# Performance work log

Measured on AMD Instinct MI355X. Metric: run time of the kernel, lower is better.

## Reference

```python
import jax, jax.numpy as jnp
import numpy as np

N_NODES = 50000
N_EDGES = 800000
IN_FEATS = 256
H_FEATS = 256
NUM_CLASSES = 16
NUM_GRAPHS = 64


def _glorot(key, shape):
    lim = float(np.sqrt(6.0 / (shape[0] + shape[1])))
    return jax.random.uniform(key, shape, jnp.float32, -lim, lim)


def setup_inputs() -> dict:
    key = jax.random.key(0)
    ks = jax.random.split(key, 12)
    x = jax.random.normal(ks[0], (N_NODES, IN_FEATS), jnp.float32)
    edge_index = jax.random.randint(ks[1], (2, N_EDGES), 0, N_NODES, jnp.int64)
    batch_vec = jnp.sort(jax.random.randint(ks[2], (N_NODES,), 0, NUM_GRAPHS, jnp.int64))
    W1 = _glorot(ks[3], (IN_FEATS, H_FEATS)); b1 = jnp.zeros((H_FEATS,), jnp.float32)
    W2 = _glorot(ks[4], (H_FEATS, H_FEATS)); b2 = jnp.zeros((H_FEATS,), jnp.float32)
    W3 = _glorot(ks[5], (H_FEATS, H_FEATS)); b3 = jnp.zeros((H_FEATS,), jnp.float32)
    W4 = _glorot(ks[6], (H_FEATS, NUM_CLASSES)); b4 = jnp.zeros((NUM_CLASSES,), jnp.float32)
    return {"x": x, "edge_index": edge_index, "batch_vec": batch_vec,
            "W1": W1, "b1": b1, "W2": W2, "b2": b2,
            "W3": W3, "b3": b3, "W4": W4, "b4": b4}


def gcn_conv(x, W, b, src, dst, deg_inv_sqrt):
    # PyG GCNConv: out = D^{-1/2} (A + I) D^{-1/2} (x W) + b
    h = x @ W  # [N, F_out]
    norm = deg_inv_sqrt[src] * deg_inv_sqrt[dst]  # [E+N]
    msgs = h[src] * norm[:, None]  # gather + scale
    agg = jax.ops.segment_sum(msgs, dst, num_segments=x.shape[0])
    return agg + b


def reference(x, edge_index, batch_vec, W1, b1, W2, b2, W3, b3, W4, b4):
    n = x.shape[0]
    # add self-loops once (shared across layers)
    loops = jnp.arange(n, dtype=edge_index.dtype)
    src = jnp.concatenate([edge_index[0], loops])
    dst = jnp.concatenate([edge_index[1], loops])
    deg = jax.ops.segment_sum(jnp.ones_like(dst, dtype=x.dtype), dst, num_segments=n)
    deg_inv_sqrt = jnp.where(deg > 0, jax.lax.rsqrt(deg), 0.0)

    h = gcn_conv(x, W1, b1, src, dst, deg_inv_sqrt)
    h_copy = jax.nn.relu(h)
    # dropout is identity in eval mode (training=False)
    h = gcn_conv(h_copy, W2, b2, src, dst, deg_inv_sqrt)
    h_copy = jax.nn.relu(jax.nn.relu(h) + h_copy)
    h = gcn_conv(h_copy, W3, b3, src, dst, deg_inv_sqrt)
    h = jax.nn.relu(jax.nn.relu(h) + h_copy)
    h = gcn_conv(h, W4, b4, src, dst, deg_inv_sqrt)

    # global_mean_pool over batch vector
    sums = jax.ops.segment_sum(h, batch_vec, num_segments=NUM_GRAPHS)
    counts = jax.ops.segment_sum(jnp.ones((n,), h.dtype), batch_vec, num_segments=NUM_GRAPHS)
    return sums / jnp.maximum(counts, 1.0)[:, None]
```

## Files before the change

kernel.cpp:

```cpp
#include <hip/hip_runtime.h>
#include <hip/hip_bf16.h>

#define N_NODES 50000
#define N_EDGES 800000
#define F 256
#define NGRAPH 64
#define NCLS 16
#define NBLK_N 196

typedef short short8 __attribute__((ext_vector_type(8)));
typedef float f32x4 __attribute__((ext_vector_type(4)));

__device__ __forceinline__ float bf2f(ushort u) {
    unsigned v = ((unsigned)u) << 16;
    return __uint_as_float(v);
}
__device__ __forceinline__ ushort f2bf(float f) {
    __hip_bfloat16 b = __float2bfloat16(f);
    return *reinterpret_cast<ushort*>(&b);
}
__device__ __forceinline__ float bflo(uint u) { return __uint_as_float(u << 16); }
__device__ __forceinline__ float bfhi(uint u) { return __uint_as_float(u & 0xffff0000u); }


__global__ __launch_bounds__(256) void k_init(int* __restrict__ ecnt,
                                              float* __restrict__ pool,
                                              float* __restrict__ cnt) {
    int i = blockIdx.x * 256 + threadIdx.x;
    if (i < N_NODES) ecnt[i] = 0;
    if (i < NGRAPH * NCLS) pool[i] = 0.f;
    if (i < NGRAPH) cnt[i] = 0.f;
}

__global__ __launch_bounds__(256) void k_count(const int* __restrict__ dst,
                                               int* __restrict__ ecnt) {
    int e = blockIdx.x * 256 + threadIdx.x;
    if (e < N_EDGES) atomicAdd(&ecnt[dst[e]], 1);
}

__global__ __launch_bounds__(256) void k_scan_block(const int* __restrict__ ecnt,
                                                    int* __restrict__ rowptr,
                                                    int* __restrict__ blkSum,
                                                    float* __restrict__ dinv,
                                                    float* __restrict__ sdeg) {
    __shared__ int sh[256];
    int i = blockIdx.x * 256 + threadIdx.x;
    int v = (i < N_NODES) ? ecnt[i] : 0;
    sh[threadIdx.x] = v;
    __syncthreads();
#pragma unroll
    for (int off = 1; off < 256; off <<= 1) {
        int t = (threadIdx.x >= off) ? sh[threadIdx.x - off] : 0;
        __syncthreads();
        sh[threadIdx.x] += t;
        __syncthreads();
    }
    if (i < N_NODES) {
        rowptr[i] = sh[threadIdx.x] - v;
        float d = (float)(v + 1);
        dinv[i] = rsqrtf(d);
        sdeg[i] = sqrtf(d);
    }
    if (threadIdx.x == 255) blkSum[blockIdx.x] = sh[255];
}

__global__ __launch_bounds__(256) void k_scan_add(const int* __restrict__ blkSum,
                                                  int* __restrict__ rowptr,
                                                  int* __restrict__ cursor) {
    __shared__ int sh[256];
    int t = threadIdx.x;
    sh[t] = (t < NBLK_N && t < (int)blockIdx.x) ? blkSum[t] : 0;
    __syncthreads();
#pragma unroll
    for (int off = 128; off > 0; off >>= 1) {
        if (t < off) sh[t] += sh[t + off];
        __syncthreads();
    }
    int base = sh[0];
    int i = blockIdx.x * 256 + t;
    if (i < N_NODES) {
        int r = rowptr[i] + base;
        rowptr[i] = r;
        cursor[i] = r;
    }
    if (i == 0) rowptr[N_NODES] = N_EDGES;
}

__global__ __launch_bounds__(256) void k_fill_csr(const int* __restrict__ src,
                                                  const int* __restrict__ dst,
                                                  int* __restrict__ cursor,
                                                  ushort* __restrict__ csr16) {
    int e = blockIdx.x * 256 + threadIdx.x;
    if (e >= N_EDGES) return;
    int s = src[e];
    int d = dst[e];
    int p = atomicAdd(&cursor[d], 1);
    csr16[p] = (ushort)s;
}


__global__ __launch_bounds__(256) void k_prescale(const float* __restrict__ x,
                                                  const float* __restrict__ dinv,
                                                  ushort* __restrict__ T0) {
    int i = blockIdx.x * 256 + threadIdx.x;
    if (i >= (int)((size_t)N_NODES * F / 8)) return;
    int n = i >> 5;
    float di = dinv[n];
    const float4* ip = (const float4*)(x + (size_t)i * 8);
    float4 a = ip[0], b = ip[1];
    short8 v;
    v[0] = (short)f2bf(a.x * di); v[1] = (short)f2bf(a.y * di);
    v[2] = (short)f2bf(a.z * di); v[3] = (short)f2bf(a.w * di);
    v[4] = (short)f2bf(b.x * di); v[5] = (short)f2bf(b.y * di);
    v[6] = (short)f2bf(b.z * di); v[7] = (short)f2bf(b.w * di);
    *(short8*)(T0 + (size_t)i * 8) = v;
}


__global__ __launch_bounds__(256) void k_wpack3(const float* __restrict__ W1,
                                                const float* __restrict__ W2,
                                                const float* __restrict__ W3,
                                                ushort* __restrict__ Wp) {
    int gid = blockIdx.x * 256 + threadIdx.x;
    int which = gid >> 13;
    int idx = gid & 8191;
    const float* W = (which == 0) ? W1 : (which == 1) ? W2 : W3;
    ushort* o = Wp + (size_t)which * 65536;
    int lane = idx & 63;
    int ks = (idx >> 6) & 7;
    int ctg = idx >> 9;
    int kbase = ks * 32 + (lane >> 4) * 8;
    int col = ctg * 16 + (lane & 15);
    short8 v;
#pragma unroll
    for (int e = 0; e < 8; ++e)
        v[e] = (short)f2bf(W[(size_t)(kbase + e) * 256 + col]);
    *(short8*)(o + (size_t)idx * 8) = v;
}


template <int MODE>
__global__ __launch_bounds__(256) void k_layer(const ushort* __restrict__ Hs,
                                               const ushort* __restrict__ Wp,
                                               const float* __restrict__ bias,
                                               const float* __restrict__ dinv,
                                               const float* __restrict__ sdeg,
                                               const int* __restrict__ rowptr,
                                               const ushort* __restrict__ csr16,
                                               ushort* __restrict__ OUT) {
    __shared__ __align__(16) ushort At[16 * 264];
    __shared__ __align__(16) ushort cs[4][16 * 72];
    const int t = threadIdx.x;
    const int wv = t >> 6;
    const int l = t & 63;
    const int m0 = blockIdx.x * 16;

    {
        const int slot = l >> 5;
        const int c = (l & 31) * 8;
#pragma unroll
        for (int rep = 0; rep < 4; ++rep) {
            const int noderow = wv * 4 + rep;
            const int n = m0 + noderow;
            const bool valid = n < N_NODES;
            const int nn = valid ? n : 0;

            float acc[8];
#pragma unroll
            for (int j = 0; j < 8; ++j) acc[j] = 0.f;

            int i = valid ? rowptr[nn] + slot : 0;
            const int end = valid ? rowptr[nn + 1] : 0;
            for (; i + 6 < end; i += 8) {
                int s0 = csr16[i], s1 = csr16[i + 2], s2 = csr16[i + 4], s3 = csr16[i + 6];
                short8 v0 = *(const short8*)(Hs + (size_t)s0 * F + c);
                short8 v1 = *(const short8*)(Hs + (size_t)s1 * F + c);
                short8 v2 = *(const short8*)(Hs + (size_t)s2 * F + c);
                short8 v3 = *(const short8*)(Hs + (size_t)s3 * F + c);
#pragma unroll
                for (int j = 0; j < 8; ++j)
                    acc[j] += (bf2f((ushort)v0[j]) + bf2f((ushort)v1[j])) +
                              (bf2f((ushort)v2[j]) + bf2f((ushort)v3[j]));
            }
            for (; i < end; i += 2) {
                int s0 = csr16[i];
                short8 v0 = *(const short8*)(Hs + (size_t)s0 * F + c);
#pragma unroll
                for (int j = 0; j < 8; ++j) acc[j] += bf2f((ushort)v0[j]);
            }

#pragma unroll
            for (int j = 0; j < 8; ++j) acc[j] += __shfl_xor(acc[j], 32);

            if (slot == 0) {
                short8 av;
                if (valid) {
                    const short8 h = *(const short8*)(Hs + (size_t)nn * F + c);
                    float di = dinv[nn];
#pragma unroll
                    for (int j = 0; j < 8; ++j)
                        av[j] = (short)f2bf(di * (acc[j] + bf2f((ushort)h[j])));
                } else {
#pragma unroll
                    for (int j = 0; j < 8; ++j) av[j] = 0;
                }
                *(short8*)&At[noderow * 264 + c] = av;
            }
        }
    }
    __syncthreads();

    const int colbase = wv * 64;
    const int lrow = l & 15;
    const int lk = (l >> 4) * 8;
    const short8* wp = (const short8*)Wp;

    short8 af[8];
#pragma unroll
    for (int ks = 0; ks < 8; ++ks)
        af[ks] = *(const short8*)&At[lrow * 264 + lk + ks * 32];

#pragma unroll
    for (int ct = 0; ct < 4; ++ct) {
        short8 wf[8];
#pragma unroll
        for (int ks = 0; ks < 8; ++ks)
            wf[ks] = wp[(size_t)(((wv * 4 + ct) * 8 + ks) * 64) + l];

        f32x4 acc = (f32x4){0.f, 0.f, 0.f, 0.f};
#pragma unroll
        for (int ks = 0; ks < 8; ++ks)
            acc = __builtin_amdgcn_mfma_f32_16x16x32_bf16(af[ks], wf[ks], acc, 0, 0, 0);

        int col = ct * 16 + (l & 15);
#pragma unroll
        for (int r = 0; r < 4; ++r) {
            int row = (l >> 4) * 4 + r;
            cs[wv][row * 72 + col] = f2bf(acc[r]);
        }
    }
#pragma unroll
    for (int h = 0; h < 2; ++h) {
        int row = h * 8 + (l >> 3);
        int coff = (l & 7) * 8;
        int orow = m0 + row;
        if (orow < N_NODES) {
            short8 z8 = *(const short8*)&cs[wv][row * 72 + coff];
            int gcol = colbase + coff;
            const float4 b0 = *(const float4*)(bias + gcol);
            const float4 b1 = *(const float4*)(bias + gcol + 4);
            float bb[8] = {b0.x, b0.y, b0.z, b0.w, b1.x, b1.y, b1.z, b1.w};
            float di = dinv[orow];
            short8 ov;
            if (MODE == 2) {
                const short8 hp = *(const short8*)(Hs + (size_t)orow * F + gcol);
                float sd = sdeg[orow];
#pragma unroll
                for (int j = 0; j < 8; ++j) {
                    float u = fmaxf(bf2f((ushort)z8[j]) + bb[j], 0.f);
                    u = fmaxf(u + bf2f((ushort)hp[j]) * sd, 0.f);
                    ov[j] = (short)f2bf(u * di);
                }
            } else {
#pragma unroll
                for (int j = 0; j < 8; ++j) {
                    float u = fmaxf(bf2f((ushort)z8[j]) + bb[j], 0.f);
                    ov[j] = (short)f2bf(u * di);
                }
            }
            *(short8*)(OUT + (size_t)orow * F + gcol) = ov;
        }
    }
}


__global__ __launch_bounds__(256) void k_gemm16(const ushort* __restrict__ A,
                                                const float* __restrict__ W4,
                                                ushort* __restrict__ C) {
    __shared__ float Ws[256][16];
    const int t = threadIdx.x;
    {
        const float4* wp = (const float4*)(W4 + (size_t)t * 16);
        float4 a = wp[0], b = wp[1], c = wp[2], d = wp[3];
        float4* sp = (float4*)&Ws[t][0];
        sp[0] = a; sp[1] = b; sp[2] = c; sp[3] = d;
    }
    __syncthreads();
    int row = blockIdx.x * 256 + t;
    if (row >= N_NODES) return;
    const short8* ap = (const short8*)(A + (size_t)row * F);
    float acc[16];
#pragma unroll
    for (int c = 0; c < 16; ++c) acc[c] = 0.f;
    for (int k8 = 0; k8 < 32; ++k8) {
        short8 a8 = ap[k8];
#pragma unroll
        for (int j = 0; j < 8; ++j) {
            float av = bf2f((ushort)a8[j]);
            const float4* wr = (const float4*)&Ws[k8 * 8 + j][0];
            float4 w0 = wr[0], w1 = wr[1], w2 = wr[2], w3 = wr[3];
            acc[0]  += av * w0.x; acc[1]  += av * w0.y;
            acc[2]  += av * w0.z; acc[3]  += av * w0.w;
            acc[4]  += av * w1.x; acc[5]  += av * w1.y;
            acc[6]  += av * w1.z; acc[7]  += av * w1.w;
            acc[8]  += av * w2.x; acc[9]  += av * w2.y;
            acc[10] += av * w2.z; acc[11] += av * w2.w;
            acc[12] += av * w3.x; acc[13] += av * w3.y;
            acc[14] += av * w3.z; acc[15] += av * w3.w;
        }
    }
    short8 o0, o1;
#pragma unroll
    for (int c = 0; c < 8; ++c) o0[c] = (short)f2bf(acc[c]);
#pragma unroll
    for (int c = 0; c < 8; ++c) o1[c] = (short)f2bf(acc[8 + c]);
    short8* op = (short8*)(C + (size_t)row * 16);
    op[0] = o0; op[1] = o1;
}


__global__ __launch_bounds__(256) void k_g16pool(const ushort* __restrict__ G16,
                                                 const float* __restrict__ bias,
                                                 const float* __restrict__ dinv,
                                                 const int* __restrict__ rowptr,
                                                 const ushort* __restrict__ csr16,
                                                 const int* __restrict__ batch,
                                                 float* __restrict__ pool,
                                                 float* __restrict__ cnt) {
    __shared__ float ps[NGRAPH][NCLS];
    __shared__ float pc[NGRAPH];
    for (int i = threadIdx.x; i < NGRAPH * NCLS; i += 256) ((float*)ps)[i] = 0.f;
    if (threadIdx.x < NGRAPH) pc[threadIdx.x] = 0.f;
    __syncthreads();

    int gid = blockIdx.x * 256 + threadIdx.x;
    int n = gid >> 2;
    int q = (gid & 3) * 4;
    if (n < N_NODES) {
        float ax = 0.f, ay = 0.f, az = 0.f, aw = 0.f;
        const int end = rowptr[n + 1];
        for (int i = rowptr[n]; i < end; ++i) {
            int s0 = csr16[i];
            const uint2 u = *(const uint2*)(G16 + (size_t)s0 * 16 + q);
            ax += bflo(u.x); ay += bfhi(u.x);
            az += bflo(u.y); aw += bfhi(u.y);
        }
        const uint2 hu = *(const uint2*)(G16 + (size_t)n * 16 + q);
        const float4 b = *(const float4*)(bias + q);
        float di = dinv[n];
        int g = batch[n];
        atomicAdd(&ps[g][q + 0], b.x + di * (ax + bflo(hu.x)));
        atomicAdd(&ps[g][q + 1], b.y + di * (ay + bfhi(hu.x)));
        atomicAdd(&ps[g][q + 2], b.z + di * (az + bflo(hu.y)));
        atomicAdd(&ps[g][q + 3], b.w + di * (aw + bfhi(hu.y)));
        if ((gid & 3) == 0) atomicAdd(&pc[g], 1.f);
    }
    __syncthreads();

    for (int i = threadIdx.x; i < NGRAPH * NCLS; i += 256) {
        float v = ((float*)ps)[i];
        if (v != 0.f) unsafeAtomicAdd(&pool[i], v);
    }
    if (threadIdx.x < NGRAPH) {
        float v = pc[threadIdx.x];
        if (v > 0.f) unsafeAtomicAdd(&cnt[threadIdx.x], v);
    }
}

__global__ __launch_bounds__(256) void k_final(const float* __restrict__ pool,
                                               const float* __restrict__ cnt,
                                               float* __restrict__ out) {
    int i = blockIdx.x * 256 + threadIdx.x;
    if (i < NGRAPH * NCLS) out[i] = pool[i] / fmaxf(cnt[i >> 4], 1.f);
}


extern "C" void kernel_launch(void* const* d_in, const int* in_sizes, int n_in,
                              void* d_out, int out_size, void* d_ws, size_t ws_size,
                              hipStream_t stream) {
    const float* x   = (const float*)d_in[0];
    const int*   ei  = (const int*)d_in[1];
    const int*   bvec= (const int*)d_in[2];
    const float* W1  = (const float*)d_in[3];
    const float* b1  = (const float*)d_in[4];
    const float* W2  = (const float*)d_in[5];
    const float* b2  = (const float*)d_in[6];
    const float* W3  = (const float*)d_in[7];
    const float* b3  = (const float*)d_in[8];
    const float* W4  = (const float*)d_in[9];
    const float* b4  = (const float*)d_in[10];
    float* out = (float*)d_out;

    const int* src = ei;
    const int* dst = ei + N_EDGES;

    const size_t NF = (size_t)N_NODES * F;
    ushort* T0  = (ushort*)d_ws;
    ushort* T1  = T0 + NF;
    ushort* T2  = T1 + NF;
    ushort* G16 = T2 + NF;
    float*  aux = (float*)(G16 + (size_t)N_NODES * 16 + 64);
    int*    ecnt   = (int*)aux;
    float*  dinv   = aux + N_NODES;
    float*  sdeg   = aux + 2 * N_NODES;
    int*    rowptr = (int*)(aux + 3 * N_NODES);
    int*    cursor = (int*)(aux + 4 * N_NODES + 64);
    int*    blkSum = (int*)(aux + 5 * N_NODES + 64);
    ushort* csr16  = (ushort*)(blkSum + 256);
    float*  pool   = (float*)(csr16 + N_EDGES);
    float*  cnt    = pool + NGRAPH * NCLS;
    ushort* Wp     = (ushort*)(cnt + NGRAPH);

    const int BN = NBLK_N;
    const int BE = (N_EDGES + 255) / 256;
    const int BL = (N_NODES + 15) / 16;
    const int B4 = (N_NODES * 4 + 255) / 256;
    const int BP = (int)((NF / 8 + 255) / 256);

    k_init<<<BN, 256, 0, stream>>>(ecnt, pool, cnt);
    k_count<<<BE, 256, 0, stream>>>(dst, ecnt);
    k_scan_block<<<BN, 256, 0, stream>>>(ecnt, rowptr, blkSum, dinv, sdeg);
    k_scan_add<<<BN, 256, 0, stream>>>(blkSum, rowptr, cursor);
    k_fill_csr<<<BE, 256, 0, stream>>>(src, dst, cursor, csr16);

    k_wpack3<<<96, 256, 0, stream>>>(W1, W2, W3, Wp);
    k_prescale<<<BP, 256, 0, stream>>>(x, dinv, T0);

    k_layer<1><<<BL, 256, 0, stream>>>(T0, Wp,          b1, dinv, sdeg, rowptr, csr16, T1);
    k_layer<2><<<BL, 256, 0, stream>>>(T1, Wp + 65536,  b2, dinv, sdeg, rowptr, csr16, T2);
    k_layer<2><<<BL, 256, 0, stream>>>(T2, Wp + 131072, b3, dinv, sdeg, rowptr, csr16, T0);

    k_gemm16<<<BN, 256, 0, stream>>>(T0, W4, G16);
    k_g16pool<<<B4, 256, 0, stream>>>(G16, b4, dinv, rowptr, csr16, bvec, pool, cnt);

    k_final<<<4, 256, 0, stream>>>(pool, cnt, out);
}
```

Baseline: 375.1 us.

## Fuse final 256x16 GEMM into third layer kernel using MFMA

The third GCN layer kernel now keeps its output tile in shared memory and multiplies it by a prepacked bf16 W4 with a 16x16x32 MFMA. It writes only the 16-wide G16 result, so the separate k_gemm16 kernel and its full write and reread of the 50000x256 activation are no longer needed. W4 is packed into MFMA layout alongside the other weights. The cost is an extra barrier, and a single wave per block does the small GEMM.

```diff
diff --git a/kernel.cpp b/kernel.cpp
--- a/kernel.cpp
+++ b/kernel.cpp
@@ -117,25 +117,40 @@
 }
 
 
-__global__ __launch_bounds__(256) void k_wpack3(const float* __restrict__ W1,
-                                                const float* __restrict__ W2,
-                                                const float* __restrict__ W3,
-                                                ushort* __restrict__ Wp) {
+__global__ __launch_bounds__(256) void k_wpack(const float* __restrict__ W1,
+                                               const float* __restrict__ W2,
+                                               const float* __restrict__ W3,
+                                               const float* __restrict__ W4,
+                                               ushort* __restrict__ Wp,
+                                               ushort* __restrict__ Wp4) {
     int gid = blockIdx.x * 256 + threadIdx.x;
-    int which = gid >> 13;
-    int idx = gid & 8191;
-    const float* W = (which == 0) ? W1 : (which == 1) ? W2 : W3;
-    ushort* o = Wp + (size_t)which * 65536;
-    int lane = idx & 63;
-    int ks = (idx >> 6) & 7;
-    int ctg = idx >> 9;
-    int kbase = ks * 32 + (lane >> 4) * 8;
-    int col = ctg * 16 + (lane & 15);
-    short8 v;
-#pragma unroll
-    for (int e = 0; e < 8; ++e)
-        v[e] = (short)f2bf(W[(size_t)(kbase + e) * 256 + col]);
-    *(short8*)(o + (size_t)idx * 8) = v;
+    if (gid < 24576) {
+        int which = gid >> 13;
+        int idx = gid & 8191;
+        const float* W = (which == 0) ? W1 : (which == 1) ? W2 : W3;
+        ushort* o = Wp + (size_t)which * 65536;
+        int lane = idx & 63;
+        int ks = (idx >> 6) & 7;
+        int ctg = idx >> 9;
+        int kbase = ks * 32 + (lane >> 4) * 8;
+        int col = ctg * 16 + (lane & 15);
+        short8 v;
+#pragma unroll
+        for (int e = 0; e < 8; ++e)
+            v[e] = (short)f2bf(W[(size_t)(kbase + e) * 256 + col]);
+        *(short8*)(o + (size_t)idx * 8) = v;
+    } else if (gid < 24576 + 512) {
+        int idx = gid - 24576;
+        int lane = idx & 63;
+        int ks = idx >> 6;
+        int kbase = ks * 32 + (lane >> 4) * 8;
+        int col = lane & 15;
+        short8 v;
+#pragma unroll
+        for (int e = 0; e < 8; ++e)
+            v[e] = (short)f2bf(W4[(size_t)(kbase + e) * 16 + col]);
+        *(short8*)(Wp4 + (size_t)idx * 8) = v;
+    }
 }
 
 
@@ -147,7 +162,9 @@
                                                const float* __restrict__ sdeg,
                                                const int* __restrict__ rowptr,
                                                const ushort* __restrict__ csr16,
-                                               ushort* __restrict__ OUT) {
+                                               ushort* __restrict__ OUT,
+                                               const ushort* __restrict__ Wp4,
+                                               ushort* __restrict__ G16) {
     __shared__ __align__(16) ushort At[16 * 264];
     __shared__ __align__(16) ushort cs[4][16 * 72];
     const int t = threadIdx.x;
@@ -252,7 +269,7 @@
             float bb[8] = {b0.x, b0.y, b0.z, b0.w, b1.x, b1.y, b1.z, b1.w};
             float di = dinv[orow];
             short8 ov;
-            if (MODE == 2) {
+            if (MODE >= 2) {
                 const short8 hp = *(const short8*)(Hs + (size_t)orow * F + gcol);
                 float sd = sdeg[orow];
 #pragma unroll
@@ -268,54 +285,41 @@
                     ov[j] = (short)f2bf(u * di);
                 }
             }
-            *(short8*)(OUT + (size_t)orow * F + gcol) = ov;
+            if (MODE == 3) {
+                *(short8*)&cs[wv][row * 72 + coff] = ov;
+            } else {
+                *(short8*)(OUT + (size_t)orow * F + gcol) = ov;
+            }
+        } else if (MODE == 3) {
+            short8 zv;
+#pragma unroll
+            for (int j = 0; j < 8; ++j) zv[j] = 0;
+            *(short8*)&cs[wv][row * 72 + coff] = zv;
         }
     }
-}
-
-
-__global__ __launch_bounds__(256) void k_gemm16(const ushort* __restrict__ A,
-                                                const float* __restrict__ W4,
-                                                ushort* __restrict__ C) {
-    __shared__ float Ws[256][16];
-    const int t = threadIdx.x;
-    {
-        const float4* wp = (const float4*)(W4 + (size_t)t * 16);
-        float4 a = wp[0], b = wp[1], c = wp[2], d = wp[3];
-        float4* sp = (float4*)&Ws[t][0];
-        sp[0] = a; sp[1] = b; sp[2] = c; sp[3] = d;
-    }
-    __syncthreads();
-    int row = blockIdx.x * 256 + t;
-    if (row >= N_NODES) return;
-    const short8* ap = (const short8*)(A + (size_t)row * F);
-    float acc[16];
-#pragma unroll
-    for (int c = 0; c < 16; ++c) acc[c] = 0.f;
-    for (int k8 = 0; k8 < 32; ++k8) {
-        short8 a8 = ap[k8];
-#pragma unroll
-        for (int j = 0; j < 8; ++j) {
-            float av = bf2f((ushort)a8[j]);
-            const float4* wr = (const float4*)&Ws[k8 * 8 + j][0];
-            float4 w0 = wr[0], w1 = wr[1], w2 = wr[2], w3 = wr[3];
-            acc[0]  += av * w0.x; acc[1]  += av * w0.y;
-            acc[2]  += av * w0.z; acc[3]  += av * w0.w;
-            acc[4]  += av * w1.x; acc[5]  += av * w1.y;
-            acc[6]  += av * w1.z; acc[7]  += av * w1.w;
-            acc[8]  += av * w2.x; acc[9]  += av * w2.y;
-            acc[10] += av * w2.z; acc[11] += av * w2.w;
-            acc[12] += av * w3.x; acc[13] += av * w3.y;
-            acc[14] += av * w3.z; acc[15] += av * w3.w;
+
+    if (MODE == 3) {
+        __syncthreads();
+        if (wv == 0) {
+            const short8* wp4 = (const short8*)Wp4;
+            f32x4 acc = (f32x4){0.f, 0.f, 0.f, 0.f};
+#pragma unroll
+            for (int ks = 0; ks < 8; ++ks) {
+                int cbase = lk + ks * 32;
+                short8 a2 = *(const short8*)&cs[cbase >> 6][lrow * 72 + (cbase & 63)];
+                short8 w4 = wp4[(size_t)(ks * 64) + l];
+                acc = __builtin_amdgcn_mfma_f32_16x16x32_bf16(a2, w4, acc, 0, 0, 0);
+            }
+            int col = l & 15;
+#pragma unroll
+            for (int r = 0; r < 4; ++r) {
+                int row = (l >> 4) * 4 + r;
+                int orow = m0 + row;
+                if (orow < N_NODES)
+                    G16[(size_t)orow * 16 + col] = f2bf(acc[r]);
+            }
         }
     }
-    short8 o0, o1;
-#pragma unroll
-    for (int c = 0; c < 8; ++c) o0[c] = (short)f2bf(acc[c]);
-#pragma unroll
-    for (int c = 0; c < 8; ++c) o1[c] = (short)f2bf(acc[8 + c]);
-    short8* op = (short8*)(C + (size_t)row * 16);
-    op[0] = o0; op[1] = o1;
 }
 
 
@@ -410,6 +414,7 @@
     float*  pool   = (float*)(csr16 + N_EDGES);
     float*  cnt    = pool + NGRAPH * NCLS;
     ushort* Wp     = (ushort*)(cnt + NGRAPH);
+    ushort* Wp4    = Wp + 3 * 65536;
 
     const int BN = NBLK_N;
     const int BE = (N_EDGES + 255) / 256;
@@ -423,14 +428,13 @@
     k_scan_add<<<BN, 256, 0, stream>>>(blkSum, rowptr, cursor);
     k_fill_csr<<<BE, 256, 0, stream>>>(src, dst, cursor, csr16);
 
-    k_wpack3<<<96, 256, 0, stream>>>(W1, W2, W3, Wp);
+    k_wpack<<<99, 256, 0, stream>>>(W1, W2, W3, W4, Wp, Wp4);
     k_prescale<<<BP, 256, 0, stream>>>(x, dinv, T0);
 
-    k_layer<1><<<BL, 256, 0, stream>>>(T0, Wp,          b1, dinv, sdeg, rowptr, csr16, T1);
-    k_layer<2><<<BL, 256, 0, stream>>>(T1, Wp + 65536,  b2, dinv, sdeg, rowptr, csr16, T2);
-    k_layer<2><<<BL, 256, 0, stream>>>(T2, Wp + 131072, b3, dinv, sdeg, rowptr, csr16, T0);
-
-    k_gemm16<<<BN, 256, 0, stream>>>(T0, W4, G16);
+    k_layer<1><<<BL, 256, 0, stream>>>(T0, Wp,          b1, dinv, sdeg, rowptr, csr16, T1, nullptr, nullptr);
+    k_layer<2><<<BL, 256, 0, stream>>>(T1, Wp + 65536,  b2, dinv, sdeg, rowptr, csr16, T2, nullptr, nullptr);
+    k_layer<3><<<BL, 256, 0, stream>>>(T2, Wp + 131072, b3, dinv, sdeg, rowptr, csr16, nullptr, Wp4, G16);
+
     k_g16pool<<<B4, 256, 0, stream>>>(G16, b4, dinv, rowptr, csr16, bvec, pool, cnt);
 
     k_final<<<4, 256, 0, stream>>>(pool, cnt, out);
```

New measurement: 353.6 us (median of 2 runs). -5.7%, faster.
